# Kernel optimization log

Measured on AMD Instinct MI355X. Metric: run time of the kernel, lower is better.

Reference implementation:

```python
import jax, jax.numpy as jnp
import numpy as np

B, L, D = 2, 4096, 128      # batch, seq_len, d_model
ED = 2 * D                  # d_inner (expand=2) = 256
N = 16                      # d_state
K = 4                       # d_conv
R = (D + 15) // 16          # dt_rank = 8
H = 2 * D                   # mlp hidden = 256


def setup_inputs() -> dict:
    key = jax.random.key(0)
    ks = jax.random.split(key, 20)
    s = 0.05
    inp = {
        "x": jax.random.normal(ks[0], (B, L, D), dtype=jnp.float32),
        # outer block LayerNorm (norm1)
        "norm1_g": jnp.ones((D,), jnp.float32),
        "norm1_b": jnp.zeros((D,), jnp.float32),
        # MambaLayer inner LayerNorm
        "inner_g": jnp.ones((D,), jnp.float32),
        "inner_b": jnp.zeros((D,), jnp.float32),
        # Mamba params
        "in_w": jax.random.normal(ks[1], (2 * ED, D), jnp.float32) * s,      # in_proj (no bias)
        "conv_w": jax.random.normal(ks[2], (ED, 1, K), jnp.float32) * s,     # depthwise conv
        "conv_b": jax.random.normal(ks[3], (ED,), jnp.float32) * s,
        "xproj_w": jax.random.normal(ks[4], (R + 2 * N, ED), jnp.float32) * s,  # x_proj (no bias)
        "dt_w": jax.random.normal(ks[5], (ED, R), jnp.float32) * s,
        "dt_b": jax.random.normal(ks[6], (ED,), jnp.float32) * s,
        "A_log": jnp.tile(jnp.log(jnp.arange(1, N + 1, dtype=jnp.float32)), (ED, 1)),  # [ED,N]
        "Dp": jnp.ones((ED,), jnp.float32),
        "out_w": jax.random.normal(ks[7], (D, ED), jnp.float32) * s,         # out_proj (no bias)
        # MLP
        "fc1_w": jax.random.normal(ks[8], (H, D), jnp.float32) * s,
        "fc1_b": jnp.zeros((H,), jnp.float32),
        "fc2_w": jax.random.normal(ks[9], (D, H), jnp.float32) * s,
        "fc2_b": jnp.zeros((D,), jnp.float32),
    }
    return inp


def _ln(x, g, b, eps=1e-5):
    m = jnp.mean(x, axis=-1, keepdims=True)
    v = jnp.mean((x - m) ** 2, axis=-1, keepdims=True)
    return (x - m) * jax.lax.rsqrt(v + eps) * g + b


def _mamba(x, in_w, conv_w, conv_b, xproj_w, dt_w, dt_b, A_log, Dp, out_w):
    # x: [B, L, D]
    xz = jnp.einsum('bld,ed->ble', x, in_w)          # [B,L,2*ED]
    u, z = jnp.split(xz, 2, axis=-1)                 # each [B,L,ED]
    # causal depthwise conv1d over L
    u_c = jnp.transpose(u, (0, 2, 1))                # [B,ED,L]
    u_c = jax.lax.conv_general_dilated(
        u_c, conv_w, window_strides=(1,), padding=[(K - 1, 0)],
        dimension_numbers=('NCH', 'OIH', 'NCH'), feature_group_count=ED)
    u = jax.nn.silu(jnp.transpose(u_c, (0, 2, 1)) + conv_b)   # [B,L,ED]
    # input-dependent dt, B, C
    dbc = jnp.einsum('ble,re->blr', u, xproj_w)      # [B,L,R+2N]
    dt, Bm, Cm = jnp.split(dbc, [R, R + N], axis=-1)
    delta = jax.nn.softplus(jnp.einsum('blr,er->ble', dt, dt_w) + dt_b)  # [B,L,ED]
    A = -jnp.exp(A_log)                              # [ED,N]
    deltaA = jnp.exp(jnp.einsum('ble,en->blen', delta, A))               # [B,L,ED,N]
    deltaBu = jnp.einsum('ble,bln,ble->blen', delta, Bm, u)              # [B,L,ED,N]
    # selective scan over L
    def step(h, inp):
        dA, dBu, Ct = inp                            # [B,ED,N],[B,ED,N],[B,N]
        h = dA * h + dBu
        y = jnp.einsum('ben,bn->be', h, Ct)
        return h, y
    h0 = jnp.zeros((B, ED, N), u.dtype)
    xs = (jnp.transpose(deltaA, (1, 0, 2, 3)),
          jnp.transpose(deltaBu, (1, 0, 2, 3)),
          jnp.transpose(Cm, (1, 0, 2)))
    _, ys = jax.lax.scan(step, h0, xs)               # [L,B,ED]
    y = jnp.transpose(ys, (1, 0, 2)) + u * Dp        # [B,L,ED]
    y = y * jax.nn.silu(z)
    return jnp.einsum('ble,de->bld', y, out_w)       # [B,L,D]


def reference(x, norm1_g, norm1_b, inner_g, inner_b, in_w, conv_w, conv_b,
              xproj_w, dt_w, dt_b, A_log, Dp, out_w, fc1_w, fc1_b, fc2_w, fc2_b):
    # attn branch: mamba(inner_LN(norm1(x)))
    a = _mamba(_ln(_ln(x, norm1_g, norm1_b), inner_g, inner_b),
               in_w, conv_w, conv_b, xproj_w, dt_w, dt_b, A_log, Dp, out_w)
    x = x + a
    # mlp branch (note: original applies norm1 again to updated x)
    h = _ln(x, norm1_g, norm1_b)
    h = jax.nn.gelu(jnp.einsum('bld,hd->blh', h, fc1_w) + fc1_b, approximate=False)
    h = jnp.einsum('blh,dh->bld', h, fc2_w) + fc2_b
    return x + h
```

## Files before the change

kernel.cpp:

```cpp
#include <hip/hip_runtime.h>
#include <hip/hip_bf16.h>
#include <math.h>

#define BB 2
#define LL 4096
#define DD 128
#define ED 256
#define NN 16
#define KK 4
#define RR 8
#define HH 256
#define NT (BB*LL)
#define NC 128
#define LC 32

typedef __attribute__((ext_vector_type(8))) short short8;
typedef __attribute__((ext_vector_type(8))) unsigned short ushort8v;
typedef __attribute__((ext_vector_type(4))) float floatx4;

__device__ __forceinline__ unsigned short f2bf(float f) {
  unsigned int b = __builtin_bit_cast(unsigned int, f);
  b += 0x7FFFu + ((b >> 16) & 1u);
  return (unsigned short)(b >> 16);
}

__device__ __forceinline__ ushort8v pack8(const float4& v0, const float4& v1) {
  ushort8v p;
  p[0]=f2bf(v0.x); p[1]=f2bf(v0.y); p[2]=f2bf(v0.z); p[3]=f2bf(v0.w);
  p[4]=f2bf(v1.x); p[5]=f2bf(v1.y); p[6]=f2bf(v1.z); p[7]=f2bf(v1.w);
  return p;
}

__global__ __launch_bounds__(256) void gemm_inln_k(const float* __restrict__ x,
    const float* __restrict__ g1, const float* __restrict__ b1,
    const float* __restrict__ g2, const float* __restrict__ b2,
    const float* __restrict__ W, float* __restrict__ C) {
  __shared__ unsigned short As[64][136];
  __shared__ unsigned short Ws[64][136];
  const int row0 = blockIdx.y * 64;
  const int col0 = blockIdx.x * 64;
  const int tid  = threadIdx.x;
  const int wave = tid >> 6, lane = tid & 63;
  const int quad = lane >> 4, l16 = lane & 15;
  const int wm = (wave & 1) * 32, wn = (wave >> 1) * 32;
  const int lr = tid >> 2;
  const int lk = (tid & 3) * 32;

  {
    const float* Ap = x + (size_t)(row0 + lr)*DD + lk;
    float4 av[8];
    float s = 0.f, sq = 0.f;
    #pragma unroll
    for (int g = 0; g < 8; g++) {
      av[g] = *(const float4*)(Ap + g*4);
      s  += av[g].x + av[g].y + av[g].z + av[g].w;
      sq += av[g].x*av[g].x + av[g].y*av[g].y + av[g].z*av[g].z + av[g].w*av[g].w;
    }
    s += __shfl_xor(s, 1);  s += __shfl_xor(s, 2);
    sq += __shfl_xor(sq, 1); sq += __shfl_xor(sq, 2);
    const float m1 = s * (1.f/128.f);
    const float rs1 = rsqrtf(sq*(1.f/128.f) - m1*m1 + 1e-5f);
    float s2 = 0.f, sq2 = 0.f;
    #pragma unroll
    for (int g = 0; g < 8; g++) {
      const float4 gg = *(const float4*)(g1 + lk + g*4);
      const float4 bb = *(const float4*)(b1 + lk + g*4);
      av[g].x = (av[g].x - m1)*rs1*gg.x + bb.x;
      av[g].y = (av[g].y - m1)*rs1*gg.y + bb.y;
      av[g].z = (av[g].z - m1)*rs1*gg.z + bb.z;
      av[g].w = (av[g].w - m1)*rs1*gg.w + bb.w;
      s2  += av[g].x + av[g].y + av[g].z + av[g].w;
      sq2 += av[g].x*av[g].x + av[g].y*av[g].y + av[g].z*av[g].z + av[g].w*av[g].w;
    }
    s2 += __shfl_xor(s2, 1);  s2 += __shfl_xor(s2, 2);
    sq2 += __shfl_xor(sq2, 1); sq2 += __shfl_xor(sq2, 2);
    const float m2 = s2 * (1.f/128.f);
    const float rs2 = rsqrtf(sq2*(1.f/128.f) - m2*m2 + 1e-5f);
    #pragma unroll
    for (int g = 0; g < 4; g++) {
      const float4 ga = *(const float4*)(g2 + lk + g*8);
      const float4 gb = *(const float4*)(g2 + lk + g*8 + 4);
      const float4 ba = *(const float4*)(b2 + lk + g*8);
      const float4 bbv= *(const float4*)(b2 + lk + g*8 + 4);
      ushort8v pa;
      pa[0] = f2bf((av[2*g].x   - m2)*rs2*ga.x + ba.x);
      pa[1] = f2bf((av[2*g].y   - m2)*rs2*ga.y + ba.y);
      pa[2] = f2bf((av[2*g].z   - m2)*rs2*ga.z + ba.z);
      pa[3] = f2bf((av[2*g].w   - m2)*rs2*ga.w + ba.w);
      pa[4] = f2bf((av[2*g+1].x - m2)*rs2*gb.x + bbv.x);
      pa[5] = f2bf((av[2*g+1].y - m2)*rs2*gb.y + bbv.y);
      pa[6] = f2bf((av[2*g+1].z - m2)*rs2*gb.z + bbv.z);
      pa[7] = f2bf((av[2*g+1].w - m2)*rs2*gb.w + bbv.w);
      *(ushort8v*)&As[lr][lk + g*8] = pa;
    }
  }
  {
    const float* Wp = W + (size_t)(col0 + lr)*DD + lk;
    #pragma unroll
    for (int g = 0; g < 4; g++) {
      const float4 v0 = *(const float4*)(Wp + g*8);
      const float4 v1 = *(const float4*)(Wp + g*8 + 4);
      *(ushort8v*)&Ws[lr][lk + g*8] = pack8(v0, v1);
    }
  }
  __syncthreads();

  floatx4 acc[2][2] = {};
  #pragma unroll
  for (int ks = 0; ks < 4; ks++) {
    const int ko = ks*32 + quad*8;
    short8 a0 = *(const short8*)&As[wm +      l16][ko];
    short8 a1 = *(const short8*)&As[wm + 16 + l16][ko];
    short8 b0 = *(const short8*)&Ws[wn +      l16][ko];
    short8 b1 = *(const short8*)&Ws[wn + 16 + l16][ko];
    acc[0][0] = __builtin_amdgcn_mfma_f32_16x16x32_bf16(a0, b0, acc[0][0], 0, 0, 0);
    acc[0][1] = __builtin_amdgcn_mfma_f32_16x16x32_bf16(a0, b1, acc[0][1], 0, 0, 0);
    acc[1][0] = __builtin_amdgcn_mfma_f32_16x16x32_bf16(a1, b0, acc[1][0], 0, 0, 0);
    acc[1][1] = __builtin_amdgcn_mfma_f32_16x16x32_bf16(a1, b1, acc[1][1], 0, 0, 0);
  }
  #pragma unroll
  for (int i = 0; i < 2; i++)
    #pragma unroll
    for (int j = 0; j < 2; j++) {
      const int n = col0 + wn + j*16 + l16;
      #pragma unroll
      for (int r = 0; r < 4; r++) {
        const int m = row0 + wm + i*16 + quad*4 + r;
        C[(size_t)m*(2*ED) + n] = acc[i][j][r];
      }
    }
}

__global__ __launch_bounds__(256) void scan1f_k(
    const float* __restrict__ xz, const float* __restrict__ cw,
    const float* __restrict__ cb, const float* __restrict__ xpw,
    const float* __restrict__ dtw, const float* __restrict__ dtb,
    const float* __restrict__ A_log, float* __restrict__ uc,
    float* __restrict__ dbc, float* __restrict__ delta,
    float* __restrict__ cA, float* __restrict__ cH) {
  __shared__ __align__(16) unsigned short Bs[64][264];
  __shared__ __align__(16) unsigned short As[32][264];
  __shared__ float su[32][128];
  __shared__ float sdbc[32][40];
  float (*sdel)[128] = reinterpret_cast<float(*)[128]>(&As[0][0]);

  const int eb = blockIdx.x, c = blockIdx.y, b = blockIdx.z;
  const int tid = threadIdx.x;
  const int t0 = b*LL + c*LC;

  #pragma unroll
  for (int p = 0; p < 8; p++) {
    const int idx = p*256 + tid;
    const int row = idx >> 5;
    const int col = (idx & 31) * 8;
    ushort8v v = {};
    if (row < 40) {
      const float4 v0 = *(const float4*)(xpw + (size_t)row*ED + col);
      const float4 v1 = *(const float4*)(xpw + (size_t)row*ED + col + 4);
      v = pack8(v0, v1);
    }
    *(ushort8v*)&Bs[row][col] = v;
  }

  {
    const int ch = tid;
    const float4 w = *(const float4*)(cw + ch*4);
    const float cbe = cb[ch];
    float h0 = 0.f, h1 = 0.f, h2 = 0.f;
    if (c != 0) {
      h0 = xz[(size_t)(t0-3)*(2*ED) + ch];
      h1 = xz[(size_t)(t0-2)*(2*ED) + ch];
      h2 = xz[(size_t)(t0-1)*(2*ED) + ch];
    }
    const bool own = (ch >> 7) == eb;
    #pragma unroll 8
    for (int i = 0; i < LC; i++) {
      const float cur = xz[(size_t)(t0+i)*(2*ED) + ch];
      const float a = cbe + h0*w.x + h1*w.y + h2*w.z + cur*w.w;
      const float s = a / (1.f + __expf(-a));
      As[i][ch] = f2bf(s);
      if (own) {
        su[i][ch & 127] = s;
        uc[(size_t)(t0+i)*ED + ch] = s;
      }
      h0 = h1; h1 = h2; h2 = cur;
    }
  }
  __syncthreads();

  const int wave = tid >> 6, lane = tid & 63;
  const int quad = lane >> 4, l16 = lane & 15;
  {
    const int mi = (wave & 1) * 16;
    const int j0 = (wave >> 1) * 2;
    floatx4 acc[2] = {};
    #pragma unroll
    for (int ks = 0; ks < 8; ks++) {
      const int ko = ks*32 + quad*8;
      short8 a  = *(const short8*)&As[mi + l16][ko];
      short8 b0 = *(const short8*)&Bs[j0*16 +      l16][ko];
      short8 b1 = *(const short8*)&Bs[j0*16 + 16 + l16][ko];
      acc[0] = __builtin_amdgcn_mfma_f32_16x16x32_bf16(a, b0, acc[0], 0, 0, 0);
      acc[1] = __builtin_amdgcn_mfma_f32_16x16x32_bf16(a, b1, acc[1], 0, 0, 0);
    }
    __syncthreads();
    #pragma unroll
    for (int f = 0; f < 2; f++) {
      const int n = (j0 + f)*16 + l16;
      #pragma unroll
      for (int r = 0; r < 4; r++) {
        const int m = mi + quad*4 + r;
        if (n < 40) {
          sdbc[m][n] = acc[f][r];
          if (eb == 0) dbc[(size_t)(t0 + m)*40 + n] = acc[f][r];
        }
      }
    }
  }
  __syncthreads();

  const int e_loc = tid >> 1;
  const int half  = tid & 1;
  const int e     = eb*128 + e_loc;
  {
    const float4 w0 = *(const float4*)(dtw + e*RR);
    const float4 w1 = *(const float4*)(dtw + e*RR + 4);
    const float db = dtb[e];
    #pragma unroll 4
    for (int i = 0; i < 16; i++) {
      const int t = half*16 + i;
      const float a = db
          + sdbc[t][0]*w0.x + sdbc[t][1]*w0.y + sdbc[t][2]*w0.z + sdbc[t][3]*w0.w
          + sdbc[t][4]*w1.x + sdbc[t][5]*w1.y + sdbc[t][6]*w1.z + sdbc[t][7]*w1.w;
      const float d = (a > 20.f) ? a : log1pf(__expf(a));
      sdel[t][e_loc] = d;
      delta[(size_t)(t0+t)*ED + e] = d;
    }
  }
  __syncthreads();

  const int n0 = half * 8;
  const float4 a0 = *(const float4*)(A_log + e*NN + n0);
  const float4 a1 = *(const float4*)(A_log + e*NN + n0 + 4);
  float Aen[8] = {-__expf(a0.x), -__expf(a0.y), -__expf(a0.z), -__expf(a0.w),
                  -__expf(a1.x), -__expf(a1.y), -__expf(a1.z), -__expf(a1.w)};
  float h[8] = {};
  float sumd = 0.f;
  for (int i = 0; i < LC; i++) {
    const float dv = sdel[i][e_loc];
    const float du = dv * su[i][e_loc];
    const float4 B0 = *(const float4*)&sdbc[i][RR + n0];
    const float4 B1 = *(const float4*)&sdbc[i][RR + n0 + 4];
    const float Bv[8] = {B0.x,B0.y,B0.z,B0.w,B1.x,B1.y,B1.z,B1.w};
    sumd += dv;
    #pragma unroll
    for (int j = 0; j < 8; j++)
      h[j] = __expf(dv * Aen[j])*h[j] + Bv[j]*du;
  }
  const size_t base = (((size_t)c*BB + b)*ED + e)*NN + n0;
  *(float4*)(cA + base)     = make_float4(__expf(sumd*Aen[0]), __expf(sumd*Aen[1]),
                                          __expf(sumd*Aen[2]), __expf(sumd*Aen[3]));
  *(float4*)(cA + base + 4) = make_float4(__expf(sumd*Aen[4]), __expf(sumd*Aen[5]),
                                          __expf(sumd*Aen[6]), __expf(sumd*Aen[7]));
  *(float4*)(cH + base)     = make_float4(h[0], h[1], h[2], h[3]);
  *(float4*)(cH + base + 4) = make_float4(h[4], h[5], h[6], h[7]);
}

__global__ __launch_bounds__(256) void scan2_k(float* __restrict__ cA,
    const float* __restrict__ cH) {
  const int gt = blockIdx.x*256 + threadIdx.x;
  const int b = gt >> 12;
  const size_t base = (size_t)b*ED*NN + (gt & 4095);
  float h = 0.f;
  for (int g = 0; g < NC/16; g++) {
    float av[16], hv[16];
    #pragma unroll
    for (int i = 0; i < 16; i++) {
      const size_t idx = (size_t)(g*16 + i)*(BB*ED*NN) + base;
      av[i] = cA[idx]; hv[i] = cH[idx];
    }
    #pragma unroll
    for (int i = 0; i < 16; i++) {
      const size_t idx = (size_t)(g*16 + i)*(BB*ED*NN) + base;
      cA[idx] = h;
      h = av[i]*h + hv[i];
    }
  }
}

__global__ __launch_bounds__(256, 2) void tail2_k(
    const float* __restrict__ xz, const float* __restrict__ delta,
    const float* __restrict__ uc, const float* __restrict__ dbc,
    const float* __restrict__ cP, const float* __restrict__ A_log,
    const float* __restrict__ Dpv, const float* __restrict__ x,
    const float* __restrict__ g1, const float* __restrict__ b1,
    const float* __restrict__ out_w, const float* __restrict__ fc1_w,
    const float* __restrict__ fc1_b, const float* __restrict__ fc2_w,
    const float* __restrict__ fc2_b, float* __restrict__ out) {
  __shared__ __align__(16) unsigned short BigW[128*136];
  __shared__ __align__(16) unsigned short Au[16][264];
  __shared__ float xs[16][132];
  __shared__ float sbc[32][32];

  const int c2 = blockIdx.x, b = blockIdx.y;
  const int c = c2 >> 1, odd = c2 & 1;
  const int tc0 = b*LL + c*LC;
  const int t0  = b*LL + c2*16;
  const int tid = threadIdx.x;
  const int wave = tid >> 6, lane = tid & 63;
  const int quad = lane >> 4, l16 = lane & 15;
  const int wn = wave * 32;

  #pragma unroll
  for (int p = 0; p < 4; p++) {
    const int idx = p*256 + tid;
    const int row = idx >> 5, col = idx & 31;
    sbc[row][col] = dbc[(size_t)(tc0 + row)*40 + RR + col];
  }

  {
    const int e = tid;
    float Aen[16], h[16];
    #pragma unroll
    for (int g = 0; g < 4; g++) {
      const float4 a = *(const float4*)(A_log + e*NN + g*4);
      Aen[4*g]=-__expf(a.x); Aen[4*g+1]=-__expf(a.y);
      Aen[4*g+2]=-__expf(a.z); Aen[4*g+3]=-__expf(a.w);
      const float4 hp = *(const float4*)(cP + (((size_t)c*BB + b)*ED + e)*NN + g*4);
      h[4*g]=hp.x; h[4*g+1]=hp.y; h[4*g+2]=hp.z; h[4*g+3]=hp.w;
    }
    const float Dpe = Dpv[e];
    __syncthreads();
    if (odd) {
      #pragma unroll 4
      for (int i = 0; i < 16; i++) {
        const float dv = delta[(size_t)(tc0+i)*ED + e];
        const float du = dv * uc[(size_t)(tc0+i)*ED + e];
        #pragma unroll
        for (int j = 0; j < 16; j++)
          h[j] = __expf(dv * Aen[j])*h[j] + sbc[i][j]*du;
      }
    }
    const int ib = odd * 16;
    #pragma unroll 4
    for (int i = 0; i < 16; i++) {
      const float dv = delta[(size_t)(t0+i)*ED + e];
      const float uv = uc[(size_t)(t0+i)*ED + e];
      const float du = dv * uv;
      float part = 0.f;
      #pragma unroll
      for (int j = 0; j < 16; j++) {
        h[j] = __expf(dv * Aen[j])*h[j] + sbc[ib+i][j]*du;
        part += h[j]*sbc[ib+i][16+j];
      }
      const float zv = xz[(size_t)(t0+i)*(2*ED) + ED + e];
      const float g = zv / (1.f + __expf(-zv));
      Au[i][e] = f2bf((part + uv*Dpe) * g);
    }
  }

  {
    floatx4 acc[2] = {};
    for (int ks0 = 0; ks0 < ED; ks0 += 128) {
      __syncthreads();
      const int r = tid >> 1, k0 = (tid & 1) * 64;
      const float* wp = out_w + (size_t)r*ED + ks0 + k0;
      #pragma unroll
      for (int g = 0; g < 8; g++) {
        const float4 v0 = *(const float4*)(wp + g*8);
        const float4 v1 = *(const float4*)(wp + g*8 + 4);
        *(ushort8v*)&BigW[r*136 + k0 + g*8] = pack8(v0, v1);
      }
      __syncthreads();
      #pragma unroll
      for (int ks = 0; ks < 4; ks++) {
        const int ko = ks*32 + quad*8;
        short8 a  = *(const short8*)&Au[l16][ks0 + ko];
        short8 b0 = *(const short8*)&BigW[(wn +      l16)*136 + ko];
        short8 b1 = *(const short8*)&BigW[(wn + 16 + l16)*136 + ko];
        acc[0] = __builtin_amdgcn_mfma_f32_16x16x32_bf16(a, b0, acc[0], 0, 0, 0);
        acc[1] = __builtin_amdgcn_mfma_f32_16x16x32_bf16(a, b1, acc[1], 0, 0, 0);
      }
    }
    #pragma unroll
    for (int j = 0; j < 2; j++) {
      const int n = wn + j*16 + l16;
      #pragma unroll
      for (int r = 0; r < 4; r++) {
        const int m = quad*4 + r;
        xs[m][n] = acc[j][r] + x[(size_t)(t0 + m)*DD + n];
      }
    }
  }
  __syncthreads();

  {
    const int lr = tid >> 4, le = (tid & 15) * 8;
    float vv[8];
    float s = 0.f, sq = 0.f;
    #pragma unroll
    for (int i = 0; i < 8; i++) {
      vv[i] = xs[lr][le + i];
      s += vv[i]; sq += vv[i]*vv[i];
    }
    s += __shfl_xor(s, 1);  s += __shfl_xor(s, 2);
    s += __shfl_xor(s, 4);  s += __shfl_xor(s, 8);
    sq += __shfl_xor(sq, 1); sq += __shfl_xor(sq, 2);
    sq += __shfl_xor(sq, 4); sq += __shfl_xor(sq, 8);
    const float mean = s * (1.f/128.f);
    const float rs = rsqrtf(sq*(1.f/128.f) - mean*mean + 1e-5f);
    ushort8v p;
    #pragma unroll
    for (int i = 0; i < 8; i++)
      p[i] = f2bf((vv[i] - mean)*rs*g1[le + i] + b1[le + i]);
    *(ushort8v*)&Au[lr][le] = p;
  }

  for (int hh = 1; hh >= 0; hh--) {
    __syncthreads();
    const int rr = tid >> 1, k0 = (tid & 1) * 64;
    const float* wp = fc1_w + (size_t)(hh*128 + rr)*DD + k0;
    #pragma unroll
    for (int g = 0; g < 8; g++) {
      const float4 v0 = *(const float4*)(wp + g*8);
      const float4 v1 = *(const float4*)(wp + g*8 + 4);
      *(ushort8v*)&BigW[rr*136 + k0 + g*8] = pack8(v0, v1);
    }
    __syncthreads();
    floatx4 acc[2] = {};
    #pragma unroll
    for (int ks = 0; ks < 4; ks++) {
      const int ko = ks*32 + quad*8;
      short8 a  = *(const short8*)&Au[l16][ko];
      short8 b0 = *(const short8*)&BigW[(wn +      l16)*136 + ko];
      short8 b1 = *(const short8*)&BigW[(wn + 16 + l16)*136 + ko];
      acc[0] = __builtin_amdgcn_mfma_f32_16x16x32_bf16(a, b0, acc[0], 0, 0, 0);
      acc[1] = __builtin_amdgcn_mfma_f32_16x16x32_bf16(a, b1, acc[1], 0, 0, 0);
    }
    if (hh == 0) __syncthreads();
    #pragma unroll
    for (int j = 0; j < 2; j++) {
      const int n = wn + j*16 + l16;
      const float bn = fc1_b[hh*128 + n];
      #pragma unroll
      for (int r = 0; r < 4; r++) {
        const int m = quad*4 + r;
        float v = acc[j][r] + bn;
        v = 0.5f*v*(1.f + erff(v*0.70710678118f));
        Au[m][hh*128 + n] = f2bf(v);
      }
    }
  }

  {
    floatx4 acc[2] = {};
    for (int ks0 = 0; ks0 < HH; ks0 += 128) {
      __syncthreads();
      const int r = tid >> 1, k0 = (tid & 1) * 64;
      const float* wp = fc2_w + (size_t)r*HH + ks0 + k0;
      #pragma unroll
      for (int g = 0; g < 8; g++) {
        const float4 v0 = *(const float4*)(wp + g*8);
        const float4 v1 = *(const float4*)(wp + g*8 + 4);
        *(ushort8v*)&BigW[r*136 + k0 + g*8] = pack8(v0, v1);
      }
      __syncthreads();
      #pragma unroll
      for (int ks = 0; ks < 4; ks++) {
        const int ko = ks*32 + quad*8;
        short8 a  = *(const short8*)&Au[l16][ks0 + ko];
        short8 b0 = *(const short8*)&BigW[(wn +      l16)*136 + ko];
        short8 b1 = *(const short8*)&BigW[(wn + 16 + l16)*136 + ko];
        acc[0] = __builtin_amdgcn_mfma_f32_16x16x32_bf16(a, b0, acc[0], 0, 0, 0);
        acc[1] = __builtin_amdgcn_mfma_f32_16x16x32_bf16(a, b1, acc[1], 0, 0, 0);
      }
    }
    #pragma unroll
    for (int j = 0; j < 2; j++) {
      const int n = wn + j*16 + l16;
      const float bn = fc2_b[n];
      #pragma unroll
      for (int r = 0; r < 4; r++) {
        const int m = quad*4 + r;
        out[(size_t)(t0 + m)*DD + n] = acc[j][r] + bn + xs[m][n];
      }
    }
  }
}

extern "C" void kernel_launch(void* const* d_in, const int* in_sizes, int n_in,
                              void* d_out, int out_size, void* d_ws, size_t ws_size,
                              hipStream_t stream) {
  const float* x      = (const float*)d_in[0];
  const float* n1g    = (const float*)d_in[1];
  const float* n1b    = (const float*)d_in[2];
  const float* ing    = (const float*)d_in[3];
  const float* inb    = (const float*)d_in[4];
  const float* in_w   = (const float*)d_in[5];
  const float* conv_w = (const float*)d_in[6];
  const float* conv_b = (const float*)d_in[7];
  const float* xproj_w= (const float*)d_in[8];
  const float* dt_w   = (const float*)d_in[9];
  const float* dt_b   = (const float*)d_in[10];
  const float* A_log  = (const float*)d_in[11];
  const float* Dpv    = (const float*)d_in[12];
  const float* out_w  = (const float*)d_in[13];
  const float* fc1_w  = (const float*)d_in[14];
  const float* fc1_b  = (const float*)d_in[15];
  const float* fc2_w  = (const float*)d_in[16];
  const float* fc2_b  = (const float*)d_in[17];
  float* out = (float*)d_out;

  float* ws    = (float*)d_ws;
  float* xz    = ws;
  float* uc    = xz    + (size_t)NT*2*ED;
  float* dbc   = uc    + (size_t)NT*ED;
  float* delta = dbc   + (size_t)NT*40;
  float* cAP   = delta + (size_t)NT*ED;
  float* cH    = cAP   + (size_t)NC*BB*ED*NN;

  gemm_inln_k<<<dim3(512/64, NT/64), 256, 0, stream>>>(x, n1g, n1b, ing, inb, in_w, xz);
  scan1f_k<<<dim3(2, NC, BB), 256, 0, stream>>>(xz, conv_w, conv_b, xproj_w, dt_w, dt_b,
                                                A_log, uc, dbc, delta, cAP, cH);
  scan2_k<<<(BB*ED*NN)/256, 256, 0, stream>>>(cAP, cH);
  tail2_k<<<dim3(2*NC, BB), 256, 0, stream>>>(xz, delta, uc, dbc, cAP, A_log, Dpv,
                                              x, n1g, n1b, out_w, fc1_w, fc1_b,
                                              fc2_w, fc2_b, out);
}
```

Before: 199.2 us.

## Merge tail blocks into 32-token 512-thread blocks and split scan state across lanes

The fused tail kernel now gives each 512-thread block one full 32-token chunk, instead of splitting the chunk over two 256-thread blocks. Before, the odd block re-ran the first 16 scan steps just to rebuild its starting state; that recompute is gone. Each channel's 16-entry state is split across two lanes, combined with a shuffle. The out_proj, fc1 and fc2 weights are now staged once per block as whole bf16 tiles, halving weight conversion per token. The cost is half as many blocks, a 32-step serial scan per block, and much more shared memory per block, which limits occupancy to one block.

After: 197.8 us. About the same (-0.7%).

```diff
diff --git a/kernel.cpp b/kernel.cpp
--- a/kernel.cpp
+++ b/kernel.cpp
@@ -288,7 +288,7 @@
   }
 }
 
-__global__ __launch_bounds__(256, 2) void tail2_k(
+__global__ __launch_bounds__(512, 1) void tail3_k(
     const float* __restrict__ xz, const float* __restrict__ delta,
     const float* __restrict__ uc, const float* __restrict__ dbc,
     const float* __restrict__ cP, const float* __restrict__ A_log,
@@ -297,97 +297,87 @@
     const float* __restrict__ out_w, const float* __restrict__ fc1_w,
     const float* __restrict__ fc1_b, const float* __restrict__ fc2_w,
     const float* __restrict__ fc2_b, float* __restrict__ out) {
-  __shared__ __align__(16) unsigned short BigW[128*136];
-  __shared__ __align__(16) unsigned short Au[16][264];
-  __shared__ float xs[16][132];
+  __shared__ __align__(16) unsigned short BigW[256*136];
+  __shared__ __align__(16) unsigned short Au[32][264];
+  __shared__ float xs[32][132];
   __shared__ float sbc[32][32];
 
-  const int c2 = blockIdx.x, b = blockIdx.y;
-  const int c = c2 >> 1, odd = c2 & 1;
-  const int tc0 = b*LL + c*LC;
-  const int t0  = b*LL + c2*16;
+  const int c = blockIdx.x, b = blockIdx.y;
+  const int t0 = b*LL + c*LC;
   const int tid = threadIdx.x;
   const int wave = tid >> 6, lane = tid & 63;
   const int quad = lane >> 4, l16 = lane & 15;
-  const int wn = wave * 32;
+  const int wm = (wave & 1) * 16;
+  const int wq = wave >> 1;
 
   #pragma unroll
-  for (int p = 0; p < 4; p++) {
-    const int idx = p*256 + tid;
+  for (int p = 0; p < 2; p++) {
+    const int idx = p*512 + tid;
     const int row = idx >> 5, col = idx & 31;
-    sbc[row][col] = dbc[(size_t)(tc0 + row)*40 + RR + col];
-  }
-
-  {
-    const int e = tid;
-    float Aen[16], h[16];
-    #pragma unroll
-    for (int g = 0; g < 4; g++) {
-      const float4 a = *(const float4*)(A_log + e*NN + g*4);
-      Aen[4*g]=-__expf(a.x); Aen[4*g+1]=-__expf(a.y);
-      Aen[4*g+2]=-__expf(a.z); Aen[4*g+3]=-__expf(a.w);
-      const float4 hp = *(const float4*)(cP + (((size_t)c*BB + b)*ED + e)*NN + g*4);
-      h[4*g]=hp.x; h[4*g+1]=hp.y; h[4*g+2]=hp.z; h[4*g+3]=hp.w;
-    }
+    sbc[row][col] = dbc[(size_t)(t0 + row)*40 + RR + col];
+  }
+
+  {
+    const int e = tid >> 1, half = tid & 1, n0 = half * 8;
+    const float4 a0 = *(const float4*)(A_log + e*NN + n0);
+    const float4 a1 = *(const float4*)(A_log + e*NN + n0 + 4);
+    float Aen[8] = {-__expf(a0.x), -__expf(a0.y), -__expf(a0.z), -__expf(a0.w),
+                    -__expf(a1.x), -__expf(a1.y), -__expf(a1.z), -__expf(a1.w)};
+    const size_t pbase = (((size_t)c*BB + b)*ED + e)*NN + n0;
+    const float4 h0 = *(const float4*)(cP + pbase);
+    const float4 h1 = *(const float4*)(cP + pbase + 4);
+    float h[8] = {h0.x,h0.y,h0.z,h0.w,h1.x,h1.y,h1.z,h1.w};
     const float Dpe = Dpv[e];
     __syncthreads();
-    if (odd) {
-      #pragma unroll 4
-      for (int i = 0; i < 16; i++) {
-        const float dv = delta[(size_t)(tc0+i)*ED + e];
-        const float du = dv * uc[(size_t)(tc0+i)*ED + e];
-        #pragma unroll
-        for (int j = 0; j < 16; j++)
-          h[j] = __expf(dv * Aen[j])*h[j] + sbc[i][j]*du;
-      }
-    }
-    const int ib = odd * 16;
     #pragma unroll 4
-    for (int i = 0; i < 16; i++) {
+    for (int i = 0; i < LC; i++) {
       const float dv = delta[(size_t)(t0+i)*ED + e];
       const float uv = uc[(size_t)(t0+i)*ED + e];
       const float du = dv * uv;
       float part = 0.f;
       #pragma unroll
-      for (int j = 0; j < 16; j++) {
-        h[j] = __expf(dv * Aen[j])*h[j] + sbc[ib+i][j]*du;
-        part += h[j]*sbc[ib+i][16+j];
-      }
-      const float zv = xz[(size_t)(t0+i)*(2*ED) + ED + e];
-      const float g = zv / (1.f + __expf(-zv));
-      Au[i][e] = f2bf((part + uv*Dpe) * g);
-    }
-  }
-
-  {
+      for (int j = 0; j < 8; j++) {
+        h[j] = __expf(dv * Aen[j])*h[j] + sbc[i][n0 + j]*du;
+        part += h[j]*sbc[i][16 + n0 + j];
+      }
+      part += __shfl_xor(part, 1);
+      if (half == 0) {
+        const float zv = xz[(size_t)(t0+i)*(2*ED) + ED + e];
+        const float g = zv / (1.f + __expf(-zv));
+        Au[i][e] = f2bf((part + uv*Dpe) * g);
+      }
+    }
+  }
+  {
+    const int r = tid >> 2, k0 = (tid & 3) * 64;
+    const float* wp = out_w + (size_t)r*ED + k0;
+    #pragma unroll
+    for (int g = 0; g < 8; g++) {
+      const float4 v0 = *(const float4*)(wp + g*8);
+      const float4 v1 = *(const float4*)(wp + g*8 + 4);
+      *(ushort8v*)&BigW[r*264 + k0 + g*8] = pack8(v0, v1);
+    }
+  }
+  __syncthreads();
+
+  {
+    const int wn = wq * 32;
     floatx4 acc[2] = {};
-    for (int ks0 = 0; ks0 < ED; ks0 += 128) {
-      __syncthreads();
-      const int r = tid >> 1, k0 = (tid & 1) * 64;
-      const float* wp = out_w + (size_t)r*ED + ks0 + k0;
-      #pragma unroll
-      for (int g = 0; g < 8; g++) {
-        const float4 v0 = *(const float4*)(wp + g*8);
-        const float4 v1 = *(const float4*)(wp + g*8 + 4);
-        *(ushort8v*)&BigW[r*136 + k0 + g*8] = pack8(v0, v1);
-      }
-      __syncthreads();
-      #pragma unroll
-      for (int ks = 0; ks < 4; ks++) {
-        const int ko = ks*32 + quad*8;
-        short8 a  = *(const short8*)&Au[l16][ks0 + ko];
-        short8 b0 = *(const short8*)&BigW[(wn +      l16)*136 + ko];
-        short8 b1 = *(const short8*)&BigW[(wn + 16 + l16)*136 + ko];
-        acc[0] = __builtin_amdgcn_mfma_f32_16x16x32_bf16(a, b0, acc[0], 0, 0, 0);
-        acc[1] = __builtin_amdgcn_mfma_f32_16x16x32_bf16(a, b1, acc[1], 0, 0, 0);
-      }
+    #pragma unroll
+    for (int ks = 0; ks < 8; ks++) {
+      const int ko = ks*32 + quad*8;
+      short8 a  = *(const short8*)&Au[wm + l16][ko];
+      short8 b0 = *(const short8*)&BigW[(wn +      l16)*264 + ko];
+      short8 b1 = *(const short8*)&BigW[(wn + 16 + l16)*264 + ko];
+      acc[0] = __builtin_amdgcn_mfma_f32_16x16x32_bf16(a, b0, acc[0], 0, 0, 0);
+      acc[1] = __builtin_amdgcn_mfma_f32_16x16x32_bf16(a, b1, acc[1], 0, 0, 0);
     }
     #pragma unroll
     for (int j = 0; j < 2; j++) {
       const int n = wn + j*16 + l16;
       #pragma unroll
       for (int r = 0; r < 4; r++) {
-        const int m = quad*4 + r;
+        const int m = wm + quad*4 + r;
         xs[m][n] = acc[j][r] + x[(size_t)(t0 + m)*DD + n];
       }
     }
@@ -415,65 +405,70 @@
       p[i] = f2bf((vv[i] - mean)*rs*g1[le + i] + b1[le + i]);
     *(ushort8v*)&Au[lr][le] = p;
   }
-
-  for (int hh = 1; hh >= 0; hh--) {
-    __syncthreads();
-    const int rr = tid >> 1, k0 = (tid & 1) * 64;
-    const float* wp = fc1_w + (size_t)(hh*128 + rr)*DD + k0;
+  {
+    const int r = tid >> 1, k0 = (tid & 1) * 64;
+    const float* wp = fc1_w + (size_t)r*DD + k0;
     #pragma unroll
     for (int g = 0; g < 8; g++) {
       const float4 v0 = *(const float4*)(wp + g*8);
       const float4 v1 = *(const float4*)(wp + g*8 + 4);
-      *(ushort8v*)&BigW[rr*136 + k0 + g*8] = pack8(v0, v1);
-    }
-    __syncthreads();
-    floatx4 acc[2] = {};
+      *(ushort8v*)&BigW[r*136 + k0 + g*8] = pack8(v0, v1);
+    }
+  }
+  __syncthreads();
+
+  {
+    const int wn = wq * 64;
+    floatx4 acc[4] = {};
     #pragma unroll
     for (int ks = 0; ks < 4; ks++) {
       const int ko = ks*32 + quad*8;
-      short8 a  = *(const short8*)&Au[l16][ko];
-      short8 b0 = *(const short8*)&BigW[(wn +      l16)*136 + ko];
-      short8 b1 = *(const short8*)&BigW[(wn + 16 + l16)*136 + ko];
+      short8 a = *(const short8*)&Au[wm + l16][ko];
+      #pragma unroll
+      for (int f = 0; f < 4; f++) {
+        short8 bv = *(const short8*)&BigW[(wn + f*16 + l16)*136 + ko];
+        acc[f] = __builtin_amdgcn_mfma_f32_16x16x32_bf16(a, bv, acc[f], 0, 0, 0);
+      }
+    }
+    __syncthreads();
+    #pragma unroll
+    for (int f = 0; f < 4; f++) {
+      const int n = wn + f*16 + l16;
+      const float bn = fc1_b[n];
+      #pragma unroll
+      for (int r = 0; r < 4; r++) {
+        const int m = wm + quad*4 + r;
+        float v = acc[f][r] + bn;
+        v = 0.5f*v*(1.f + erff(v*0.70710678118f));
+        Au[m][n] = f2bf(v);
+      }
+    }
+  }
+  __syncthreads();
+
+  {
+    const int r = tid >> 2, k0 = (tid & 3) * 64;
+    const float* wp = fc2_w + (size_t)r*HH + k0;
+    #pragma unroll
+    for (int g = 0; g < 8; g++) {
+      const float4 v0 = *(const float4*)(wp + g*8);
+      const float4 v1 = *(const float4*)(wp + g*8 + 4);
+      *(ushort8v*)&BigW[r*264 + k0 + g*8] = pack8(v0, v1);
+    }
+  }
+  __syncthreads();
+
+  {
+    const int wn = wq * 32;
+    floatx4 acc[2] = {};
+    #pragma unroll
+    for (int ks = 0; ks < 8; ks++) {
+      const int ko = ks*32 + quad*8;
+      short8 a  = *(const short8*)&Au[wm + l16][ko];
+      short8 b0 = *(const short8*)&BigW[(wn +      l16)*264 + ko];
+      short8 b1 = *(const short8*)&BigW[(wn + 16 + l16)*264 + ko];
       acc[0] = __builtin_amdgcn_mfma_f32_16x16x32_bf16(a, b0, acc[0], 0, 0, 0);
       acc[1] = __builtin_amdgcn_mfma_f32_16x16x32_bf16(a, b1, acc[1], 0, 0, 0);
-    }
-    if (hh == 0) __syncthreads();
-    #pragma unroll
-    for (int j = 0; j < 2; j++) {
-      const int n = wn + j*16 + l16;
-      const float bn = fc1_b[hh*128 + n];
-      #pragma unroll
-      for (int r = 0; r < 4; r++) {
-        const int m = quad*4 + r;
-        float v = acc[j][r] + bn;
-        v = 0.5f*v*(1.f + erff(v*0.70710678118f));
-        Au[m][hh*128 + n] = f2bf(v);
-      }
-    }
-  }
-
-  {
-    floatx4 acc[2] = {};
-    for (int ks0 = 0; ks0 < HH; ks0 += 128) {
-      __syncthreads();
-      const int r = tid >> 1, k0 = (tid & 1) * 64;
-      const float* wp = fc2_w + (size_t)r*HH + ks0 + k0;
-      #pragma unroll
-      for (int g = 0; g < 8; g++) {
-        const float4 v0 = *(const float4*)(wp + g*8);
-        const float4 v1 = *(const float4*)(wp + g*8 + 4);
-        *(ushort8v*)&BigW[r*136 + k0 + g*8] = pack8(v0, v1);
-      }
-      __syncthreads();
-      #pragma unroll
-      for (int ks = 0; ks < 4; ks++) {
-        const int ko = ks*32 + quad*8;
-        short8 a  = *(const short8*)&Au[l16][ks0 + ko];
-        short8 b0 = *(const short8*)&BigW[(wn +      l16)*136 + ko];
-        short8 b1 = *(const short8*)&BigW[(wn + 16 + l16)*136 + ko];
-        acc[0] = __builtin_amdgcn_mfma_f32_16x16x32_bf16(a, b0, acc[0], 0, 0, 0);
-        acc[1] = __builtin_amdgcn_mfma_f32_16x16x32_bf16(a, b1, acc[1], 0, 0, 0);
-      }
     }
     #pragma unroll
     for (int j = 0; j < 2; j++) {
@@ -481,7 +476,7 @@
       const float bn = fc2_b[n];
       #pragma unroll
       for (int r = 0; r < 4; r++) {
-        const int m = quad*4 + r;
+        const int m = wm + quad*4 + r;
         out[(size_t)(t0 + m)*DD + n] = acc[j][r] + bn + xs[m][n];
       }
     }
@@ -523,7 +518,7 @@
   scan1f_k<<<dim3(2, NC, BB), 256, 0, stream>>>(xz, conv_w, conv_b, xproj_w, dt_w, dt_b,
                                                 A_log, uc, dbc, delta, cAP, cH);
   scan2_k<<<(BB*ED*NN)/256, 256, 0, stream>>>(cAP, cH);
-  tail2_k<<<dim3(2*NC, BB), 256, 0, stream>>>(xz, delta, uc, dbc, cAP, A_log, Dpv,
-                                              x, n1g, n1b, out_w, fc1_w, fc1_b,
-                                              fc2_w, fc2_b, out);
-}
+  tail3_k<<<dim3(NC, BB), 512, 0, stream>>>(xz, delta, uc, dbc, cAP, A_log, Dpv,
+                                            x, n1g, n1b, out_w, fc1_w, fc1_b,
+                                            fc2_w, fc2_b, out);
+}
```
